# Performance work log

Measured on AMD Instinct MI355X. Metric: run time of the kernel, lower is better.

The kernel has to match this reference:

```python
import jax, jax.numpy as jnp
import numpy as np
from jax import lax

STRIDE = (1, 1)
PADDING = ((1, 1), (1, 1))


@jax.custom_vjp
def ternary_quantize(w):
    """Quantize OIHW weights to {-1,0,+1} with per-output-channel scale alpha."""
    abs_w = jnp.abs(w)
    delta = 0.7 * abs_w.mean(axis=(1, 2, 3), keepdims=True)          # [O,1,1,1]
    ternary = jnp.where(w > delta, 1.0, jnp.where(w < -delta, -1.0, 0.0)).astype(w.dtype)
    mask = ternary != 0
    count = jnp.maximum(mask.sum(axis=(1, 2, 3), keepdims=True), 1).astype(w.dtype)
    alpha = (abs_w * mask.astype(w.dtype)).sum(axis=(1, 2, 3), keepdims=True) / count
    return ternary, alpha


def _tq_fwd(w):
    return ternary_quantize(w), w


def _tq_bwd(w, grads):
    g_ternary, _g_alpha = grads  # STE: grad_alpha is discarded
    g = jnp.where(jnp.abs(w) > 1.0, 0.0, g_ternary)
    return (g,)


ternary_quantize.defvjp(_tq_fwd, _tq_bwd)


def setup_inputs() -> dict:
    key = jax.random.key(0)
    kx, kw = jax.random.split(key)
    x = jax.random.normal(kx, (32, 256, 56, 56), dtype=jnp.float32)
    # kaiming_normal fan_out: std = sqrt(2 / (out_ch * kH * kW))
    std = np.sqrt(2.0 / (256 * 3 * 3)).astype(np.float32)
    weight = jax.random.normal(kw, (256, 256, 3, 3), dtype=jnp.float32) * std
    return {"x": x, "weight": weight}


def reference(x, weight):
    ternary, alpha = ternary_quantize(weight)
    scaled_w = alpha * ternary  # values in {-alpha_o, 0, +alpha_o}
    return lax.conv_general_dilated(
        x, scaled_w,
        window_strides=STRIDE,
        padding=PADDING,
        dimension_numbers=("NCHW", "OIHW", "NCHW"),
    )
```

## Files before the change

### kernel.cpp

```cpp
#include <hip/hip_runtime.h>
#include <hip/hip_bf16.h>

typedef unsigned short u16;
typedef __bf16 bf16x8 __attribute__((ext_vector_type(8)));
typedef float f32x4 __attribute__((ext_vector_type(4)));
typedef u16 u16x8 __attribute__((ext_vector_type(8)));

__device__ __forceinline__ u16 f2bf(float f) {
    __bf16 h = (__bf16)f;
    return __builtin_bit_cast(unsigned short, h);
}

__device__ __forceinline__ void gl_lds16(const u16* g, u16* l) {
    __builtin_amdgcn_global_load_lds(
        (const __attribute__((address_space(1))) void*)g,
        (__attribute__((address_space(3))) void*)l, 16, 0, 0);
}

__global__ __launch_bounds__(256) void prep_kernel(
        const float* __restrict__ x, const float* __restrict__ w,
        u16* __restrict__ xp, u16* __restrict__ wp,
        float* __restrict__ alpha) {
    __shared__ double red[4];
    __shared__ double red2[4];
    __shared__ int    redc[4];

    int bid = blockIdx.x;
    int t = threadIdx.x;

    if (bid < 256) {
        int o = bid;
        const float* wo = w + (size_t)o * 2304;
        float v[9];
        double asum = 0.0;
        #pragma unroll
        for (int i = 0; i < 9; ++i) { v[i] = wo[t * 9 + i]; asum += fabs((double)v[i]); }
        #pragma unroll
        for (int off = 32; off > 0; off >>= 1) asum += __shfl_down(asum, off, 64);
        int wv = t >> 6, lane = t & 63;
        if (lane == 0) red[wv] = asum;
        __syncthreads();
        double delta = 0.7 * ((red[0] + red[1] + red[2] + red[3]) / 2304.0);

        int mt = o >> 7, ol = o & 127;
        int ks = (t >> 3) & 7, c = t & 7;
        double msum = 0.0; int cnt = 0;
        #pragma unroll
        for (int i = 0; i < 9; ++i) {
            double f = (double)v[i];
            float tv = 0.f;
            if (f > delta) tv = 1.f;
            else if (f < -delta) tv = -1.f;
            if (tv != 0.f) { msum += fabs(f); cnt++; }
            int kc = i * 4 + (t >> 6);
            wp[((((size_t)mt * 36 + kc) * 8 + ks) * 128 + ol) * 8 + c] = f2bf(tv);
        }
        #pragma unroll
        for (int off = 32; off > 0; off >>= 1) {
            msum += __shfl_down(msum, off, 64);
            cnt  += __shfl_down(cnt,  off, 64);
        }
        if (lane == 0) { red2[wv] = msum; redc[wv] = cnt; }
        __syncthreads();
        if (t == 0) {
            double ms = red2[0] + red2[1] + red2[2] + red2[3];
            int cn = redc[0] + redc[1] + redc[2] + redc[3];
            alpha[o] = (float)(ms / (double)(cn > 0 ? cn : 1));
        }
        return;
    }

    int pbid = bid - 256;
    int img  = pbid & 31;
    int cihi = (pbid >> 5) & 31;
    int z    = pbid >> 10;

    if (z == 3 && t >= 16) {
        int bt = t - 16;
        if (bt < 228) {
            int hp, wl;
            if (bt < 58)       { hp = 0;            wl = bt; }
            else if (bt < 116) { hp = 57;           wl = bt - 58; }
            else if (bt < 172) { hp = bt - 116 + 1; wl = 0; }
            else               { hp = bt - 172 + 1; wl = 57; }
            u16x8 zv = {};
            *(u16x8*)(xp + (((size_t)(img * 32 + cihi) * 58 + hp) * 58 + wl) * 8) = zv;
        }
        return;
    }

    int slot = z * 256 + t;
    if (slot >= 784) return;
    int p = slot * 4;
    int h = p / 56, wq = p - h * 56;
    const float* xb = x + ((size_t)(img * 256 + cihi * 8)) * 3136 + p;
    f32x4 v[8];
    #pragma unroll
    for (int j = 0; j < 8; ++j) v[j] = *(const f32x4*)(xb + (size_t)j * 3136);
    u16* ob = xp + (((size_t)(img * 32 + cihi) * 58 + (h + 1)) * 58 + (wq + 1)) * 8;
    #pragma unroll
    for (int k = 0; k < 4; ++k) {
        u16x8 ov;
        #pragma unroll
        for (int j = 0; j < 8; ++j) ov[j] = f2bf(v[j][k]);
        *(u16x8*)(ob + k * 8) = ov;
    }
}

#define STAGE_CHUNK(KC, LA, LB) do {                                        \
    int f_ = (KC) >> 2;                                                      \
    int kh_ = f_ / 3, kw_ = f_ - kh_ * 3;                                    \
    int ci8_ = ((KC) & 3) * 8;                                               \
    unsigned bhw_ = (unsigned)kh_ * 464u + (unsigned)kw_ * 8u;               \
    unsigned bo0_ = (unsigned)(ci8_ + s0) * 26912u + bhw_;                   \
    unsigned bo1_ = (unsigned)(ci8_ + s1) * 26912u + bhw_;                   \
    const u16* aC_ = aTile + (size_t)(KC) * 8192;                            \
    _Pragma("unroll")                                                        \
    for (int q_ = 0; q_ < 4; ++q_) {                                         \
        int seg_ = wave * 4 + q_;                                            \
        gl_lds16(aC_ + seg_ * 512 + lane * 8, (LA) + seg_ * 512);            \
    }                                                                        \
    gl_lds16(bB0 + bo0_, (LB) + s0 * 1024);                                  \
    gl_lds16(bB1 + bo0_, (LB) + s0 * 1024 + 512);                            \
    gl_lds16(bB0 + bo1_, (LB) + s1 * 1024);                                  \
    gl_lds16(bB1 + bo1_, (LB) + s1 * 1024 + 512);                            \
} while (0)

#define HALF_ITER(LA, LB, VMSTR, STAGE_KC, DO_STAGE) do {                    \
    asm volatile("s_waitcnt " VMSTR ::: "memory");                           \
    __builtin_amdgcn_sched_barrier(0);                                       \
    __builtin_amdgcn_s_barrier();                                            \
    __builtin_amdgcn_sched_barrier(0);                                       \
    bf16x8 af_[2][4], bf_[2][4];                                             \
    _Pragma("unroll")                                                        \
    for (int kk_ = 0; kk_ < 2; ++kk_) {                                      \
        int ks_ = kk_ * 4 + quad;                                            \
        _Pragma("unroll")                                                    \
        for (int i_ = 0; i_ < 4; ++i_)                                       \
            af_[kk_][i_] = *(const bf16x8*)&(LA)[(ks_ * 128 + wm + i_ * 16 + row16) * 8]; \
        _Pragma("unroll")                                                    \
        for (int j_ = 0; j_ < 4; ++j_)                                       \
            bf_[kk_][j_] = *(const bf16x8*)&(LB)[(ks_ * 128 + wn + j_ * 16 + row16) * 8]; \
    }                                                                        \
    __builtin_amdgcn_sched_barrier(0);                                       \
    asm volatile("s_waitcnt lgkmcnt(0)" ::: "memory");                       \
    __builtin_amdgcn_sched_barrier(0);                                       \
    __builtin_amdgcn_s_barrier();                                            \
    __builtin_amdgcn_sched_barrier(0);                                       \
    if (DO_STAGE) STAGE_CHUNK(STAGE_KC, LA, LB);                             \
    __builtin_amdgcn_s_setprio(1);                                           \
    _Pragma("unroll")                                                        \
    for (int kk_ = 0; kk_ < 2; ++kk_)                                        \
        _Pragma("unroll")                                                    \
        for (int i_ = 0; i_ < 4; ++i_)                                       \
            _Pragma("unroll")                                                \
            for (int j_ = 0; j_ < 4; ++j_)                                   \
                acc[i_][j_] = __builtin_amdgcn_mfma_f32_16x16x32_bf16(       \
                                af_[kk_][i_], bf_[kk_][j_], acc[i_][j_], 0, 0, 0); \
    __builtin_amdgcn_s_setprio(0);                                           \
} while (0)

__global__ __launch_bounds__(256, 2) void conv_gemm(
        const u16* __restrict__ Wp, const u16* __restrict__ Xp,
        const float* __restrict__ alpha, float* __restrict__ out) {
    __shared__ u16 lsA0[8 * 128 * 8];
    __shared__ u16 lsA1[8 * 128 * 8];
    __shared__ u16 lsB0[8 * 128 * 8];
    __shared__ u16 lsB1[8 * 128 * 8];

    int bid = blockIdx.x;
    int xcd = bid & 7, idx = bid >> 3;
    int mt = idx & 1;
    unsigned nt = (unsigned)(xcd * 98 + (idx >> 1));
    int o_base = mt * 128;
    unsigned sp_base = nt * 128u;

    int t = threadIdx.x;
    int lane = t & 63, wave = t >> 6;
    int wm = (wave >> 1) * 64, wn = (wave & 1) * 64;

    const u16* aTile = Wp + (size_t)mt * 294912;

    unsigned sp0 = sp_base + (unsigned)lane;
    unsigned sp1 = sp0 + 64u;
    unsigned img0 = sp0 / 3136u, rem0 = sp0 - img0 * 3136u;
    unsigned oh0 = rem0 / 56u,   ow0 = rem0 - oh0 * 56u;
    unsigned img1 = sp1 / 3136u, rem1 = sp1 - img1 * 3136u;
    unsigned oh1 = rem1 / 56u,   ow1 = rem1 - oh1 * 56u;
    const u16* bB0 = Xp + ((size_t)(img0 * 32) * 58 + oh0) * 58 * 8 + ow0 * 8;
    const u16* bB1 = Xp + ((size_t)(img1 * 32) * 58 + oh1) * 58 * 8 + ow1 * 8;

    int s0 = wave * 2, s1 = s0 + 1;

    f32x4 acc[4][4] = {};
    int row16 = lane & 15, quad = lane >> 4;

    STAGE_CHUNK(0, lsA0, lsB0);
    STAGE_CHUNK(1, lsA1, lsB1);

    #pragma unroll 1
    for (int kc = 0; kc < 34; kc += 2) {
        HALF_ITER(lsA0, lsB0, "vmcnt(8)", kc + 2, true);
        HALF_ITER(lsA1, lsB1, "vmcnt(8)", kc + 3, true);
    }
    HALF_ITER(lsA0, lsB0, "vmcnt(8)", 0, false);
    HALF_ITER(lsA1, lsB1, "vmcnt(0)", 0, false);

    int col = lane & 15;
    float al[4][4];
    #pragma unroll
    for (int i = 0; i < 4; ++i)
        #pragma unroll
        for (int rg = 0; rg < 4; ++rg)
            al[i][rg] = alpha[o_base + wm + i * 16 + quad * 4 + rg];

    #pragma unroll
    for (int j = 0; j < 4; ++j) {
        unsigned sp = sp_base + (unsigned)(wn + j * 16 + col);
        unsigned img = sp / 3136u;
        unsigned spi = sp - img * 3136u;
        float* ob = out + (size_t)img * 256 * 3136 + spi;
        #pragma unroll
        for (int i = 0; i < 4; ++i) {
            int o = o_base + wm + i * 16 + quad * 4;
            #pragma unroll
            for (int rg = 0; rg < 4; ++rg)
                ob[(size_t)(o + rg) * 3136] = acc[i][j][rg] * al[i][rg];
        }
    }
}

extern "C" void kernel_launch(void* const* d_in, const int* in_sizes, int n_in,
                              void* d_out, int out_size, void* d_ws, size_t ws_size,
                              hipStream_t stream) {
    const float* x = (const float*)d_in[0];
    const float* w = (const float*)d_in[1];
    float* out = (float*)d_out;

    char* ws = (char*)d_ws;
    u16*   xp    = (u16*)ws;
    u16*   wp    = (u16*)(ws + 55115776);
    float* alpha = (float*)(ws + 55115776 + 1179648);

    prep_kernel<<<4352, 256, 0, stream>>>(x, w, xp, wp, alpha);
    conv_gemm<<<784 * 2, 256, 0, stream>>>(wp, xp, alpha, out);
}
```

Baseline: 307.6 us.

## Double-buffer register fragments to overlap LDS reads with MFMA compute

Restructures the main GEMM loop so the LDS fragment reads for the next K-chunk are issued while the MFMAs for the current chunk run, using two register fragment sets (af0/bf0, af1/bf1). The global-to-LDS staging of the following chunk is issued at the start of each step instead of after the fragment reads. The aim is to hide LDS read latency behind matrix math instead of serialising read, wait, then compute. In exchange it uses more VGPRs for the second fragment set, which may pressure occupancy under launch_bounds(256,2), and the reordered barriers must keep the LDS reuse correct.

Result: slower. 315.8 us (+2.7%).

```diff
diff --git a/kernel.cpp b/kernel.cpp
--- a/kernel.cpp
+++ b/kernel.cpp
@@ -107,7 +107,9 @@
     }
 }
 
-#define STAGE_CHUNK(KC, LA, LB) do {                                        \
+#define SB __builtin_amdgcn_sched_barrier(0)
+
+#define STAGE_CHUNK(KC, LA, LB) do {                                         \
     int f_ = (KC) >> 2;                                                      \
     int kh_ = f_ / 3, kw_ = f_ - kh_ * 3;                                    \
     int ci8_ = ((KC) & 3) * 8;                                               \
@@ -126,28 +128,20 @@
     gl_lds16(bB1 + bo1_, (LB) + s1 * 1024 + 512);                            \
 } while (0)
 
-#define HALF_ITER(LA, LB, VMSTR, STAGE_KC, DO_STAGE) do {                    \
-    asm volatile("s_waitcnt " VMSTR ::: "memory");                           \
-    __builtin_amdgcn_sched_barrier(0);                                       \
-    __builtin_amdgcn_s_barrier();                                            \
-    __builtin_amdgcn_sched_barrier(0);                                       \
-    bf16x8 af_[2][4], bf_[2][4];                                             \
+#define READ_FRAGS(AF, BF, LA, LB) do {                                      \
     _Pragma("unroll")                                                        \
     for (int kk_ = 0; kk_ < 2; ++kk_) {                                      \
         int ks_ = kk_ * 4 + quad;                                            \
         _Pragma("unroll")                                                    \
         for (int i_ = 0; i_ < 4; ++i_)                                       \
-            af_[kk_][i_] = *(const bf16x8*)&(LA)[(ks_ * 128 + wm + i_ * 16 + row16) * 8]; \
+            AF[kk_][i_] = *(const bf16x8*)&(LA)[(ks_ * 128 + wm + i_ * 16 + row16) * 8]; \
         _Pragma("unroll")                                                    \
         for (int j_ = 0; j_ < 4; ++j_)                                       \
-            bf_[kk_][j_] = *(const bf16x8*)&(LB)[(ks_ * 128 + wn + j_ * 16 + row16) * 8]; \
+            BF[kk_][j_] = *(const bf16x8*)&(LB)[(ks_ * 128 + wn + j_ * 16 + row16) * 8]; \
     }                                                                        \
-    __builtin_amdgcn_sched_barrier(0);                                       \
-    asm volatile("s_waitcnt lgkmcnt(0)" ::: "memory");                       \
-    __builtin_amdgcn_sched_barrier(0);                                       \
-    __builtin_amdgcn_s_barrier();                                            \
-    __builtin_amdgcn_sched_barrier(0);                                       \
-    if (DO_STAGE) STAGE_CHUNK(STAGE_KC, LA, LB);                             \
+} while (0)
+
+#define MFMA_CHUNK(AF, BF) do {                                              \
     __builtin_amdgcn_s_setprio(1);                                           \
     _Pragma("unroll")                                                        \
     for (int kk_ = 0; kk_ < 2; ++kk_)                                        \
@@ -156,8 +150,24 @@
             _Pragma("unroll")                                                \
             for (int j_ = 0; j_ < 4; ++j_)                                   \
                 acc[i_][j_] = __builtin_amdgcn_mfma_f32_16x16x32_bf16(       \
-                                af_[kk_][i_], bf_[kk_][j_], acc[i_][j_], 0, 0, 0); \
+                                AF[kk_][i_], BF[kk_][j_], acc[i_][j_], 0, 0, 0); \
     __builtin_amdgcn_s_setprio(0);                                           \
+} while (0)
+
+#define PIPE_BODY(AFc, BFc, AFn, BFn, LAc, LBc, LAn, LBn, SKC) do {          \
+    STAGE_CHUNK(SKC, LAc, LBc);                                              \
+    SB;                                                                      \
+    asm volatile("s_waitcnt vmcnt(8)" ::: "memory");                         \
+    SB;                                                                      \
+    __builtin_amdgcn_s_barrier();                                            \
+    SB;                                                                      \
+    READ_FRAGS(AFn, BFn, LAn, LBn);                                          \
+    MFMA_CHUNK(AFc, BFc);                                                    \
+    SB;                                                                      \
+    asm volatile("s_waitcnt lgkmcnt(0)" ::: "memory");                       \
+    SB;                                                                      \
+    __builtin_amdgcn_s_barrier();                                            \
+    SB;                                                                      \
 } while (0)
 
 __global__ __launch_bounds__(256, 2) void conv_gemm(
@@ -195,16 +205,38 @@
     f32x4 acc[4][4] = {};
     int row16 = lane & 15, quad = lane >> 4;
 
+    bf16x8 af0[2][4], bf0[2][4];
+    bf16x8 af1[2][4], bf1[2][4];
+
     STAGE_CHUNK(0, lsA0, lsB0);
     STAGE_CHUNK(1, lsA1, lsB1);
+    SB;
+    asm volatile("s_waitcnt vmcnt(8)" ::: "memory");
+    SB;
+    __builtin_amdgcn_s_barrier();
+    SB;
+    READ_FRAGS(af0, bf0, lsA0, lsB0);
+    SB;
+    asm volatile("s_waitcnt lgkmcnt(0)" ::: "memory");
+    SB;
+    __builtin_amdgcn_s_barrier();
+    SB;
 
     #pragma unroll 1
     for (int kc = 0; kc < 34; kc += 2) {
-        HALF_ITER(lsA0, lsB0, "vmcnt(8)", kc + 2, true);
-        HALF_ITER(lsA1, lsB1, "vmcnt(8)", kc + 3, true);
-    }
-    HALF_ITER(lsA0, lsB0, "vmcnt(8)", 0, false);
-    HALF_ITER(lsA1, lsB1, "vmcnt(0)", 0, false);
+        PIPE_BODY(af0, bf0, af1, bf1, lsA0, lsB0, lsA1, lsB1, kc + 2);
+        PIPE_BODY(af1, bf1, af0, bf0, lsA1, lsB1, lsA0, lsB0, kc + 3);
+    }
+    asm volatile("s_waitcnt vmcnt(0)" ::: "memory");
+    SB;
+    __builtin_amdgcn_s_barrier();
+    SB;
+    READ_FRAGS(af1, bf1, lsA1, lsB1);
+    MFMA_CHUNK(af0, bf0);
+    SB;
+    asm volatile("s_waitcnt lgkmcnt(0)" ::: "memory");
+    SB;
+    MFMA_CHUNK(af1, bf1);
 
     int col = lane & 15;
     float al[4][4];
```
